# Kernel tuning notes

Measured on AMD Instinct MI355X. Metric: run time of the kernel, lower is better.

The kernel has to match this reference:

```python
import jax, jax.numpy as jnp
import numpy as np

B, LQ, LV, D = 16, 2048, 2048, 1024


def setup_inputs() -> dict:
    key = jax.random.key(0)
    kq, kv = jax.random.split(key)
    query = jax.random.normal(kq, (B, LQ, D), dtype=jnp.float32)
    value = jax.random.normal(kv, (B, LV, D), dtype=jnp.float32)
    return {"query": query, "value": value}


def reference(query, value):
    # score: [B, Lq, Lv] -- unscaled dot-product attention (no 1/sqrt(d))
    score = jnp.einsum('bqd,bvd->bqv', query, value)
    attn = jax.nn.softmax(score, axis=-1)
    # dropout is identity in eval mode
    context = jnp.einsum('bqv,bvd->bqd', attn, value)
    return context
```

## Files before the change

kernel.cpp:

```cpp
#include <hip/hip_runtime.h>


#define B_ 16
#define LQ_ 2048
#define LV_ 2048
#define DD_ 1024

typedef unsigned short u16;
typedef _Float16 f16x8 __attribute__((ext_vector_type(8)));
typedef __attribute__((ext_vector_type(4))) float f32x4;
typedef __attribute__((ext_vector_type(4))) unsigned short u16x4;

__device__ __forceinline__ u16 f2h(float x) {
  union { _Float16 h; u16 u; } c;
  c.h = (_Float16)x;
  return c.u;
}

__device__ __forceinline__ void gload16(const u16* g, u16* lds) {
  __builtin_amdgcn_global_load_lds(
      (const __attribute__((address_space(1))) void*)g,
      (__attribute__((address_space(3))) void*)lds, 16, 0, 0);
}

#define BARRIER() do { asm volatile("" ::: "memory"); __builtin_amdgcn_s_barrier(); asm volatile("" ::: "memory"); } while (0)
#define WAITVM(N) asm volatile("s_waitcnt vmcnt(" #N ")" ::: "memory")

template <int TPS, int MODE>
__global__ __launch_bounds__(512, 2) void k_gemm8(
    const u16* __restrict__ A, const u16* __restrict__ B,
    u16* __restrict__ Pout, float* __restrict__ Fout,
    const u16* __restrict__ r2tab, const float* __restrict__ fintab,
    float* __restrict__ mtab, float* __restrict__ stab,
    int N, int lda, int ldb, size_t aBatch, size_t bBatch, size_t cBatch) {
  constexpr int NT = TPS;
  __shared__ u16 lds[65536];
  __shared__ float red[4][256];
  __shared__ u16 ldsR2[2048];
  __shared__ float ldsFin[256];
  u16* ldsA = lds;
  u16* ldsB = lds + 32768;

  int bx, by, bz;
  {
    const int gx = gridDim.x, gy = gridDim.y;
    const int lid = blockIdx.x + gx * (blockIdx.y + gy * blockIdx.z);
    const int nwg = gx * gy * gridDim.z;
    const int q = nwg >> 3;
    const int nid = (lid & 7) * q + (lid >> 3);
    bx = nid % gx;
    const int rem = nid / gx;
    by = rem % gy;
    bz = rem / gy;
  }

  const int tid = threadIdx.x;
  const int w = tid >> 6, l = tid & 63;
  const int m0 = by << 8, n0 = bx << 8;
  const int wr = w >> 2, wc = w & 3;
  const int wr128 = wr * 128, wc64 = wc * 64;
  const int fr = l & 15, kx = l >> 4, fr7 = l & 7, cc = l & 15;
  const int srow = l >> 3;
  const int gsrc8 = (((l & 7) ^ ((l >> 3) & 7)) << 3);

  const u16* Ab = A + (size_t)bz * aBatch;
  const u16* Bb = B + (size_t)bz * bBatch;

  if constexpr (MODE == 2) {
    for (int i = tid; i < 2048; i += 512)
      ldsR2[i] = r2tab[((size_t)bz * 8 + (i >> 8)) * 2048 + m0 + (i & 255)];
    for (int i = tid; i < 256; i += 512)
      ldsFin[i] = fintab[(size_t)bz * 2048 + m0 + i];
    __syncthreads();
  }

#define STAGE_A(tt, h)                                                          \
  do {                                                                          \
    const int kk_ = (tt) * 64;                                                  \
    u16* d0_ = ldsA + ((tt) & 1) * 16384 + ((h) * 64 + w * 8) * 64;             \
    const u16* g0_ = Ab + (size_t)(m0 + (h) * 64 + w * 8 + srow) * lda + kk_ + gsrc8; \
    gload16(g0_, d0_);                                                          \
    gload16(g0_ + (size_t)128 * lda, d0_ + 128 * 64);                           \
  } while (0)

#define STAGE_B(tt, h)                                                          \
  do {                                                                          \
    const int kk_ = (tt) * 64;                                                  \
    const int rb_ = (w >> 2) * 64 + (h) * 32 + (w & 3) * 8;                     \
    u16* d0_ = ldsB + ((tt) & 1) * 16384 + rb_ * 64;                            \
    const u16* g0_ = Bb + (size_t)(n0 + rb_ + srow) * ldb + kk_ + gsrc8;        \
    gload16(g0_, d0_);                                                          \
    gload16(g0_ + (size_t)128 * ldb, d0_ + 8192);                               \
  } while (0)

#define RA8(MOFF)                                                                   \
  {                                                                                 \
    _Pragma("unroll") for (int m_ = 0; m_ < 4; ++m_) {                              \
      _Pragma("unroll") for (int k_ = 0; k_ < 2; ++k_) {                            \
        af[m_][k_] = *(const f16x8*)(ldsA + bufo +                                  \
            (wr128 + (MOFF) + m_ * 16 + fr) * 64 + (((kx + k_ * 4) ^ fr7) << 3));   \
        if constexpr (MODE == 2) af[m_][k_] = af[m_][k_] * r2h[(MOFF) / 16 + m_];   \
      }                                                                             \
    }                                                                               \
  }

#define RB4(NF0)                                                                    \
  {                                                                                 \
    _Pragma("unroll") for (int n_ = 0; n_ < 2; ++n_) {                              \
      _Pragma("unroll") for (int k_ = 0; k_ < 2; ++k_) {                            \
        bf[(NF0) + n_][k_] = *(const f16x8*)(ldsB + bufo +                          \
            (wc64 + ((NF0) + n_) * 16 + fr) * 64 + (((kx + k_ * 4) ^ fr7) << 3));   \
      }                                                                             \
    }                                                                               \
  }

#define MFMA8(MF0, NF0)                                                             \
  {                                                                                 \
    _Pragma("unroll") for (int m_ = 0; m_ < 4; ++m_)                                \
    _Pragma("unroll") for (int n_ = 0; n_ < 2; ++n_)                                \
    _Pragma("unroll") for (int k_ = 0; k_ < 2; ++k_)                                \
        acc[(MF0) + m_][(NF0) + n_] = __builtin_amdgcn_mfma_f32_16x16x32_f16(       \
            af[m_][k_], bf[(NF0) + n_][k_], acc[(MF0) + m_][(NF0) + n_], 0, 0, 0);  \
  }

  f32x4 acc[8][4];
#pragma unroll
  for (int i = 0; i < 8; ++i)
#pragma unroll
    for (int j = 0; j < 4; ++j) acc[i][j] = (f32x4){0.f, 0.f, 0.f, 0.f};
  f16x8 af[4][2], bf[4][2];
  _Float16 r2h[8];

  STAGE_A(0, 0); STAGE_A(0, 1); STAGE_B(0, 0); STAGE_B(0, 1);
  STAGE_A(1, 0); STAGE_B(1, 0); STAGE_A(1, 1);
  WAITVM(6);
  BARRIER();

#pragma unroll 2
  for (int t = 0; t < NT; ++t) {
    const int bufo = (t & 1) * 16384;
    if constexpr (MODE == 2) {
      if ((t & 3) == 0) {
        const int chb = (t >> 2) * 256;
#pragma unroll
        for (int i = 0; i < 8; ++i)
          r2h[i] = *(const _Float16*)&ldsR2[chb + wr128 + i * 16 + fr];
      }
    }
    RA8(0);
    RB4(0);
    if (t + 1 < NT) STAGE_B(t + 1, 1);
    BARRIER();
    __builtin_amdgcn_s_setprio(1); MFMA8(0, 0); __builtin_amdgcn_s_setprio(0);
    BARRIER();
    RB4(2);
    if (t + 2 < NT) STAGE_A(t + 2, 0);
    BARRIER();
    __builtin_amdgcn_s_setprio(1); MFMA8(0, 2); __builtin_amdgcn_s_setprio(0);
    BARRIER();
    RA8(64);
    if (t + 2 < NT) STAGE_B(t + 2, 0);
    BARRIER();
    __builtin_amdgcn_s_setprio(1); MFMA8(4, 0); __builtin_amdgcn_s_setprio(0);
    BARRIER();
    if (t + 2 < NT) STAGE_A(t + 2, 1);
    BARRIER();
    __builtin_amdgcn_s_setprio(1); MFMA8(4, 2); __builtin_amdgcn_s_setprio(0);
    if (t + 2 < NT) { WAITVM(6); } else if (t + 1 < NT) { WAITVM(0); }
    BARRIER();
  }

  const int rg4 = (l >> 4) * 4;
  if constexpr (MODE == 1) {
    float mt[8][4];
#pragma unroll
    for (int mf = 0; mf < 8; ++mf)
#pragma unroll
      for (int j = 0; j < 4; ++j) {
        float v = fmaxf(fmaxf(acc[mf][0][j], acc[mf][1][j]),
                        fmaxf(acc[mf][2][j], acc[mf][3][j]));
#pragma unroll
        for (int off = 1; off < 16; off <<= 1) v = fmaxf(v, __shfl_xor(v, off, 64));
        if ((l & 15) == 0) red[w & 3][wr128 + mf * 16 + rg4 + j] = v;
      }
    __syncthreads();
#pragma unroll
    for (int mf = 0; mf < 8; ++mf)
#pragma unroll
      for (int j = 0; j < 4; ++j) {
        const int r_ = wr128 + mf * 16 + rg4 + j;
        mt[mf][j] = fmaxf(fmaxf(red[0][r_], red[1][r_]), fmaxf(red[2][r_], red[3][r_]));
      }
    __syncthreads();
    u16* Pc = Pout + (size_t)bz * ((size_t)2048 * 2048);
#pragma unroll
    for (int mf = 0; mf < 8; ++mf)
#pragma unroll
      for (int j = 0; j < 4; ++j) {
        const int r_ = wr128 + mf * 16 + rg4 + j;
        float s = 0.f;
#pragma unroll
        for (int nf = 0; nf < 4; ++nf) {
          const float e = __expf(acc[mf][nf][j] - mt[mf][j]);
          s += e;
          Pc[(size_t)(m0 + r_) * 2048 + n0 + wc64 + nf * 16 + cc] = f2h(e);
        }
#pragma unroll
        for (int off = 1; off < 16; off <<= 1) s += __shfl_xor(s, off, 64);
        if ((l & 15) == 0) red[w & 3][r_] = s;
      }
    __syncthreads();
    if (((w & 3) == 0) && ((l & 15) == 0)) {
#pragma unroll
      for (int mf = 0; mf < 8; ++mf)
#pragma unroll
        for (int j = 0; j < 4; ++j) {
          const int r_ = wr128 + mf * 16 + rg4 + j;
          const float st = red[0][r_] + red[1][r_] + red[2][r_] + red[3][r_];
          mtab[((size_t)bz * 8 + bx) * 2048 + m0 + r_] = mt[mf][j];
          stab[((size_t)bz * 8 + bx) * 2048 + m0 + r_] = st;
        }
    }
  } else {
#pragma unroll
    for (int mf = 0; mf < 8; ++mf)
#pragma unroll
      for (int nf = 0; nf < 4; ++nf) {
        float* cp = Fout + (size_t)bz * cBatch +
                    (size_t)(m0 + wr128 + mf * 16 + rg4) * N + n0 + wc64 + nf * 16 + cc;
#pragma unroll
        for (int j = 0; j < 4; ++j)
          cp[(size_t)j * N] = acc[mf][nf][j] * ldsFin[wr128 + mf * 16 + rg4 + j];
      }
  }
#undef STAGE_A
#undef STAGE_B
#undef RA8
#undef RB4
#undef MFMA8
}

__global__ __launch_bounds__(256) void k_stats(const float* __restrict__ mtab,
                                               const float* __restrict__ stab,
                                               u16* __restrict__ r2tab,
                                               float* __restrict__ fintab) {
  const int r = blockIdx.x * 256 + threadIdx.x;
  const int bz = blockIdx.y;
  float m[8], s[8], mg = -3.0e38f;
#pragma unroll
  for (int t = 0; t < 8; ++t) {
    m[t] = mtab[((size_t)bz * 8 + t) * 2048 + r];
    s[t] = stab[((size_t)bz * 8 + t) * 2048 + r];
    mg = fmaxf(mg, m[t]);
  }
  float denom = 0.f;
#pragma unroll
  for (int t = 0; t < 8; ++t) {
    const float f = __expf(m[t] - mg);
    denom += s[t] * f;
    r2tab[((size_t)bz * 8 + t) * 2048 + r] = f2h(f);
  }
  fintab[(size_t)bz * 2048 + r] = 1.0f / denom;
}

__global__ __launch_bounds__(256) void k_conv_q(const float* __restrict__ in,
                                                u16* __restrict__ hi_o, int nrows) {
  int t = blockIdx.x * 256 + threadIdx.x;
  int total = nrows * (DD_ / 4);
  if (t >= total) return;
  int row = t >> 8;
  int c4 = (t & 255) << 2;
  float4 v = *(const float4*)(in + (size_t)row * DD_ + c4);
  u16x4 hi;
  hi.x = f2h(v.x);
  hi.y = f2h(v.y);
  hi.z = f2h(v.z);
  hi.w = f2h(v.w);
  *(u16x4*)(hi_o + (size_t)row * DD_ + c4) = hi;
}

__global__ __launch_bounds__(256) void k_conv_vt(const float* __restrict__ V,
                                                 u16* __restrict__ Vh,
                                                 u16* __restrict__ VT) {
  __shared__ u16 tile[64][65];
  const int d0 = blockIdx.x * 64, v0 = blockIdx.y * 64;
  const size_t boff = (size_t)blockIdx.z * LV_ * DD_;
  const float* Vb = V + boff;
  u16* Vhb = Vh + boff;
  u16* VTb = VT + (size_t)blockIdx.z * DD_ * LV_;
  const int t = threadIdx.x;
  const int r = t >> 4, c4 = (t & 15) * 4;
#pragma unroll
  for (int i = 0; i < 4; ++i) {
    int row = r + i * 16;
    float4 x = *(const float4*)(Vb + (size_t)(v0 + row) * DD_ + d0 + c4);
    u16x4 h;
    h.x = f2h(x.x);
    h.y = f2h(x.y);
    h.z = f2h(x.z);
    h.w = f2h(x.w);
    *(u16x4*)(Vhb + (size_t)(v0 + row) * DD_ + d0 + c4) = h;
    tile[row][c4 + 0] = h.x;
    tile[row][c4 + 1] = h.y;
    tile[row][c4 + 2] = h.z;
    tile[row][c4 + 3] = h.w;
  }
  __syncthreads();
#pragma unroll
  for (int i = 0; i < 4; ++i) {
    int row = r + i * 16;
    u16x4 o;
    o.x = tile[c4 + 0][row];
    o.y = tile[c4 + 1][row];
    o.z = tile[c4 + 2][row];
    o.w = tile[c4 + 3][row];
    *(u16x4*)(VTb + (size_t)(d0 + row) * LV_ + v0 + c4) = o;
  }
}

extern "C" void kernel_launch(void* const* d_in, const int* in_sizes, int n_in,
                              void* d_out, int out_size, void* d_ws, size_t ws_size,
                              hipStream_t stream) {
  const float* Q = (const float*)d_in[0];
  const float* V = (const float*)d_in[1];
  float* out = (float*)d_out;

  const size_t qv_e = (size_t)LQ_ * DD_;
  const size_t vt_e = (size_t)DD_ * LV_;
  const size_t p_e = (size_t)LQ_ * LV_;
  const size_t tab_e = (size_t)8 * 2048;
  const size_t per_batch =
      qv_e * 2 * 2 + vt_e * 2 + p_e * 2 + tab_e * 4 * 2 + tab_e * 2 + 2048 * 4;

  int nb = (int)(ws_size / per_batch);
  if (nb < 1) nb = 1;
  if (nb > B_) nb = B_;

  char* wp = (char*)d_ws;
  u16* Qh = (u16*)wp;    wp += (size_t)nb * qv_e * 2;
  u16* Vh = (u16*)wp;    wp += (size_t)nb * qv_e * 2;
  u16* VT = (u16*)wp;    wp += (size_t)nb * vt_e * 2;
  u16* P = (u16*)wp;     wp += (size_t)nb * p_e * 2;
  float* mtab = (float*)wp;  wp += (size_t)nb * tab_e * 4;
  float* stab = (float*)wp;  wp += (size_t)nb * tab_e * 4;
  u16* r2tab = (u16*)wp;     wp += (size_t)nb * tab_e * 2;
  float* fintab = (float*)wp;

  for (int b0 = 0; b0 < B_; b0 += nb) {
    const int cb = (nb < B_ - b0) ? nb : (B_ - b0);
    const int rows = cb * LQ_;
    const int cthreads = rows * (DD_ / 4);
    k_conv_q<<<dim3((cthreads + 255) / 256), dim3(256), 0, stream>>>(
        Q + (size_t)b0 * LQ_ * DD_, Qh, rows);
    k_conv_vt<<<dim3(DD_ / 64, LV_ / 64, cb), dim3(256), 0, stream>>>(
        V + (size_t)b0 * LV_ * DD_, Vh, VT);
    k_gemm8<16, 1><<<dim3(LV_ / 256, LQ_ / 256, cb), dim3(512), 0, stream>>>(
        Qh, Vh, P, nullptr, nullptr, nullptr, mtab, stab,
        LV_, DD_, DD_, qv_e, qv_e, 0);
    k_stats<<<dim3(LQ_ / 256, cb), dim3(256), 0, stream>>>(mtab, stab, r2tab, fintab);
    k_gemm8<32, 2><<<dim3(DD_ / 256, LQ_ / 256, cb), dim3(512), 0, stream>>>(
        P, VT, nullptr, out + (size_t)b0 * LQ_ * DD_, r2tab, fintab, nullptr, nullptr,
        DD_, LV_, LV_, p_e, vt_e, (size_t)LQ_ * DD_);
  }
}
```

Before: 457.3 us.

## Keep per-wave softmax stats and fold normalization into rescale factors

The QK^T epilogue no longer reduces row max and sum across the four column waves through shared memory with several block barriers. Each wave now writes its own 64-column max/sum chunk, giving 32 chunks per row instead of 8. The stats kernel merges 32 chunks and folds 1/denominator into the fp16 rescale factors, so the PV epilogue drops its final multiply and the fintab load. The cost is 4x larger stat tables, a per-iteration r2 LDS read in the second GEMM, and a larger LDS table there.

```diff
diff --git a/kernel.cpp b/kernel.cpp
--- a/kernel.cpp
+++ b/kernel.cpp
@@ -30,14 +30,12 @@
 __global__ __launch_bounds__(512, 2) void k_gemm8(
     const u16* __restrict__ A, const u16* __restrict__ B,
     u16* __restrict__ Pout, float* __restrict__ Fout,
-    const u16* __restrict__ r2tab, const float* __restrict__ fintab,
+    const u16* __restrict__ r2tab,
     float* __restrict__ mtab, float* __restrict__ stab,
     int N, int lda, int ldb, size_t aBatch, size_t bBatch, size_t cBatch) {
   constexpr int NT = TPS;
   __shared__ u16 lds[65536];
-  __shared__ float red[4][256];
-  __shared__ u16 ldsR2[2048];
-  __shared__ float ldsFin[256];
+  __shared__ u16 ldsR2[(MODE == 2) ? 8192 : 64];
   u16* ldsA = lds;
   u16* ldsB = lds + 32768;
 
@@ -67,10 +65,8 @@
   const u16* Bb = B + (size_t)bz * bBatch;
 
   if constexpr (MODE == 2) {
-    for (int i = tid; i < 2048; i += 512)
-      ldsR2[i] = r2tab[((size_t)bz * 8 + (i >> 8)) * 2048 + m0 + (i & 255)];
-    for (int i = tid; i < 256; i += 512)
-      ldsFin[i] = fintab[(size_t)bz * 2048 + m0 + i];
+    for (int i = tid; i < 8192; i += 512)
+      ldsR2[i] = r2tab[((size_t)bz * 32 + (i >> 8)) * 2048 + m0 + (i & 255)];
     __syncthreads();
   }
 
@@ -140,12 +136,9 @@
   for (int t = 0; t < NT; ++t) {
     const int bufo = (t & 1) * 16384;
     if constexpr (MODE == 2) {
-      if ((t & 3) == 0) {
-        const int chb = (t >> 2) * 256;
-#pragma unroll
-        for (int i = 0; i < 8; ++i)
-          r2h[i] = *(const _Float16*)&ldsR2[chb + wr128 + i * 16 + fr];
-      }
+#pragma unroll
+      for (int i = 0; i < 8; ++i)
+        r2h[i] = *(const _Float16*)&ldsR2[t * 256 + wr128 + i * 16 + fr];
     }
     RA8(0);
     RB4(0);
@@ -172,54 +165,39 @@
 
   const int rg4 = (l >> 4) * 4;
   if constexpr (MODE == 1) {
-    float mt[8][4];
-#pragma unroll
-    for (int mf = 0; mf < 8; ++mf)
+    u16* Pc = Pout + (size_t)bz * ((size_t)2048 * 2048);
+    const int chunk = bx * 4 + wc;
+    const size_t tbase = ((size_t)bz * 32 + chunk) * 2048 + m0;
+#pragma unroll
+    for (int mf = 0; mf < 8; ++mf) {
+      float mt4[4], st4[4];
 #pragma unroll
       for (int j = 0; j < 4; ++j) {
+        const int r_ = wr128 + mf * 16 + rg4 + j;
         float v = fmaxf(fmaxf(acc[mf][0][j], acc[mf][1][j]),
                         fmaxf(acc[mf][2][j], acc[mf][3][j]));
 #pragma unroll
         for (int off = 1; off < 16; off <<= 1) v = fmaxf(v, __shfl_xor(v, off, 64));
-        if ((l & 15) == 0) red[w & 3][wr128 + mf * 16 + rg4 + j] = v;
+        const float e0 = __expf(acc[mf][0][j] - v);
+        const float e1 = __expf(acc[mf][1][j] - v);
+        const float e2 = __expf(acc[mf][2][j] - v);
+        const float e3 = __expf(acc[mf][3][j] - v);
+        u16* pr = Pc + (size_t)(m0 + r_) * 2048 + n0 + wc64 + cc;
+        pr[0] = f2h(e0);
+        pr[16] = f2h(e1);
+        pr[32] = f2h(e2);
+        pr[48] = f2h(e3);
+        float s = (e0 + e1) + (e2 + e3);
+#pragma unroll
+        for (int off = 1; off < 16; off <<= 1) s += __shfl_xor(s, off, 64);
+        mt4[j] = v;
+        st4[j] = s;
       }
-    __syncthreads();
-#pragma unroll
-    for (int mf = 0; mf < 8; ++mf)
-#pragma unroll
-      for (int j = 0; j < 4; ++j) {
-        const int r_ = wr128 + mf * 16 + rg4 + j;
-        mt[mf][j] = fmaxf(fmaxf(red[0][r_], red[1][r_]), fmaxf(red[2][r_], red[3][r_]));
+      if ((l & 15) == 0) {
+        const int r0 = wr128 + mf * 16 + rg4;
+        *(float4*)&mtab[tbase + r0] = make_float4(mt4[0], mt4[1], mt4[2], mt4[3]);
+        *(float4*)&stab[tbase + r0] = make_float4(st4[0], st4[1], st4[2], st4[3]);
       }
-    __syncthreads();
-    u16* Pc = Pout + (size_t)bz * ((size_t)2048 * 2048);
-#pragma unroll
-    for (int mf = 0; mf < 8; ++mf)
-#pragma unroll
-      for (int j = 0; j < 4; ++j) {
-        const int r_ = wr128 + mf * 16 + rg4 + j;
-        float s = 0.f;
-#pragma unroll
-        for (int nf = 0; nf < 4; ++nf) {
-          const float e = __expf(acc[mf][nf][j] - mt[mf][j]);
-          s += e;
-          Pc[(size_t)(m0 + r_) * 2048 + n0 + wc64 + nf * 16 + cc] = f2h(e);
-        }
-#pragma unroll
-        for (int off = 1; off < 16; off <<= 1) s += __shfl_xor(s, off, 64);
-        if ((l & 15) == 0) red[w & 3][r_] = s;
-      }
-    __syncthreads();
-    if (((w & 3) == 0) && ((l & 15) == 0)) {
-#pragma unroll
-      for (int mf = 0; mf < 8; ++mf)
-#pragma unroll
-        for (int j = 0; j < 4; ++j) {
-          const int r_ = wr128 + mf * 16 + rg4 + j;
-          const float st = red[0][r_] + red[1][r_] + red[2][r_] + red[3][r_];
-          mtab[((size_t)bz * 8 + bx) * 2048 + m0 + r_] = mt[mf][j];
-          stab[((size_t)bz * 8 + bx) * 2048 + m0 + r_] = st;
-        }
     }
   } else {
 #pragma unroll
@@ -230,7 +208,7 @@
                     (size_t)(m0 + wr128 + mf * 16 + rg4) * N + n0 + wc64 + nf * 16 + cc;
 #pragma unroll
         for (int j = 0; j < 4; ++j)
-          cp[(size_t)j * N] = acc[mf][nf][j] * ldsFin[wr128 + mf * 16 + rg4 + j];
+          cp[(size_t)j * N] = acc[mf][nf][j];
       }
   }
 #undef STAGE_A
@@ -242,25 +220,27 @@
 
 __global__ __launch_bounds__(256) void k_stats(const float* __restrict__ mtab,
                                                const float* __restrict__ stab,
-                                               u16* __restrict__ r2tab,
-                                               float* __restrict__ fintab) {
+                                               u16* __restrict__ r2tab) {
   const int r = blockIdx.x * 256 + threadIdx.x;
   const int bz = blockIdx.y;
-  float m[8], s[8], mg = -3.0e38f;
-#pragma unroll
-  for (int t = 0; t < 8; ++t) {
-    m[t] = mtab[((size_t)bz * 8 + t) * 2048 + r];
-    s[t] = stab[((size_t)bz * 8 + t) * 2048 + r];
+  float m[32], s[32], mg = -3.0e38f;
+#pragma unroll
+  for (int t = 0; t < 32; ++t) {
+    m[t] = mtab[((size_t)bz * 32 + t) * 2048 + r];
+    s[t] = stab[((size_t)bz * 32 + t) * 2048 + r];
     mg = fmaxf(mg, m[t]);
   }
   float denom = 0.f;
-#pragma unroll
-  for (int t = 0; t < 8; ++t) {
-    const float f = __expf(m[t] - mg);
-    denom += s[t] * f;
-    r2tab[((size_t)bz * 8 + t) * 2048 + r] = f2h(f);
-  }
-  fintab[(size_t)bz * 2048 + r] = 1.0f / denom;
+  float f[32];
+#pragma unroll
+  for (int t = 0; t < 32; ++t) {
+    f[t] = __expf(m[t] - mg);
+    denom += s[t] * f[t];
+  }
+  const float inv = 1.0f / denom;
+#pragma unroll
+  for (int t = 0; t < 32; ++t)
+    r2tab[((size_t)bz * 32 + t) * 2048 + r] = f2h(f[t] * inv);
 }
 
 __global__ __launch_bounds__(256) void k_conv_q(const float* __restrict__ in,
@@ -328,9 +308,9 @@
   const size_t qv_e = (size_t)LQ_ * DD_;
   const size_t vt_e = (size_t)DD_ * LV_;
   const size_t p_e = (size_t)LQ_ * LV_;
-  const size_t tab_e = (size_t)8 * 2048;
+  const size_t tab_e = (size_t)32 * 2048;
   const size_t per_batch =
-      qv_e * 2 * 2 + vt_e * 2 + p_e * 2 + tab_e * 4 * 2 + tab_e * 2 + 2048 * 4;
+      qv_e * 2 * 2 + vt_e * 2 + p_e * 2 + tab_e * 4 * 2 + tab_e * 2;
 
   int nb = (int)(ws_size / per_batch);
   if (nb < 1) nb = 1;
@@ -343,8 +323,7 @@
   u16* P = (u16*)wp;     wp += (size_t)nb * p_e * 2;
   float* mtab = (float*)wp;  wp += (size_t)nb * tab_e * 4;
   float* stab = (float*)wp;  wp += (size_t)nb * tab_e * 4;
-  u16* r2tab = (u16*)wp;     wp += (size_t)nb * tab_e * 2;
-  float* fintab = (float*)wp;
+  u16* r2tab = (u16*)wp;
 
   for (int b0 = 0; b0 < B_; b0 += nb) {
     const int cb = (nb < B_ - b0) ? nb : (B_ - b0);
@@ -355,11 +334,11 @@
     k_conv_vt<<<dim3(DD_ / 64, LV_ / 64, cb), dim3(256), 0, stream>>>(
         V + (size_t)b0 * LV_ * DD_, Vh, VT);
     k_gemm8<16, 1><<<dim3(LV_ / 256, LQ_ / 256, cb), dim3(512), 0, stream>>>(
-        Qh, Vh, P, nullptr, nullptr, nullptr, mtab, stab,
+        Qh, Vh, P, nullptr, nullptr, mtab, stab,
         LV_, DD_, DD_, qv_e, qv_e, 0);
-    k_stats<<<dim3(LQ_ / 256, cb), dim3(256), 0, stream>>>(mtab, stab, r2tab, fintab);
+    k_stats<<<dim3(LQ_ / 256, cb), dim3(256), 0, stream>>>(mtab, stab, r2tab);
     k_gemm8<32, 2><<<dim3(DD_ / 256, LQ_ / 256, cb), dim3(512), 0, stream>>>(
-        P, VT, nullptr, out + (size_t)b0 * LQ_ * DD_, r2tab, fintab, nullptr, nullptr,
+        P, VT, nullptr, out + (size_t)b0 * LQ_ * DD_, r2tab, nullptr, nullptr,
         DD_, LV_, LV_, p_e, vt_e, (size_t)LQ_ * DD_);
   }
 }
```

Result: faster. 416.1 us, median of 2 (-9.0%).
